# Kernel optimization log

Hardware: AMD Instinct MI355X
Metric: run time of the kernel (lower is better)

Reference implementation:

```python
import jax, jax.numpy as jnp
import numpy as np

N = 100000
E = 1600000
D_IN = 128
D_OUT = 128
D_DEC = 2
TAU = 0.5
NEG_SLOPE = 0.2  # PyG GATv2Conv default negative_slope


def _glorot(key, shape):
    lim = (6.0 / (shape[0] + shape[1])) ** 0.5
    return jax.random.uniform(key, shape, jnp.float32, -lim, lim)


def gatv2(x, edge_index, Wl, Wr, bl, br, att, bias):
    """PyG GATv2Conv, heads=1, add_self_loops=True, eval mode (no dropout).
    out[i] = sum_j softmax_i( att . leaky_relu(xl[j] + xr[i]) ) * xl[j] + bias
    """
    n = x.shape[0]
    loops = jnp.arange(n, dtype=edge_index.dtype)
    src = jnp.concatenate([edge_index[0], loops])  # [E+N]
    dst = jnp.concatenate([edge_index[1], loops])
    xl = x @ Wl + bl  # [N, out]
    xr = x @ Wr + br
    # per-edge unnormalized score
    e = jax.nn.leaky_relu(xl[src] + xr[dst], NEG_SLOPE) @ att  # [E+N]
    # scatter-softmax over incoming edges of each target node
    m = jax.ops.segment_max(e, dst, num_segments=n)
    a = jnp.exp(e - m[dst])
    s = jax.ops.segment_sum(a, dst, num_segments=n)
    alpha = a / (s[dst] + 1e-16)
    out = jax.ops.segment_sum(alpha[:, None] * xl[src], dst, num_segments=n)
    return out + bias


def setup_inputs() -> dict:
    key = jax.random.key(0)
    ks = jax.random.split(key, 16)
    x = jax.random.normal(ks[0], (N, D_IN), jnp.float32)
    edge_dec = jax.random.randint(ks[1], (2, E), 0, N, jnp.int64)
    edge_0 = jax.random.randint(ks[2], (2, E), 0, N, jnp.int64)
    edge_1 = jax.random.randint(ks[3], (2, E), 0, N, jnp.int64)
    u = jax.random.uniform(ks[4], (N, D_DEC), jnp.float32, 1e-6, 1.0 - 1e-6)
    gumbel = -jnp.log(-jnp.log(u))  # Gumbel(0,1) noise
    # shared GAT (used for every decision branch)
    Wl_g = _glorot(ks[5], (D_IN, D_OUT))
    Wr_g = _glorot(ks[6], (D_IN, D_OUT))
    bl_g = jnp.zeros((D_OUT,), jnp.float32)
    br_g = jnp.zeros((D_OUT,), jnp.float32)
    att_g = _glorot(ks[7], (D_OUT, 1))[:, 0]
    bias_g = jnp.zeros((D_OUT,), jnp.float32)
    # decision GAT
    Wl_d = _glorot(ks[8], (D_IN, D_DEC))
    Wr_d = _glorot(ks[9], (D_IN, D_DEC))
    bl_d = jnp.zeros((D_DEC,), jnp.float32)
    br_d = jnp.zeros((D_DEC,), jnp.float32)
    att_d = _glorot(ks[10], (D_DEC, 1))[:, 0]
    bias_d = jnp.zeros((D_DEC,), jnp.float32)
    return {"x": x, "edge_dec": edge_dec, "edge_0": edge_0, "edge_1": edge_1,
            "gumbel": gumbel,
            "Wl_g": Wl_g, "Wr_g": Wr_g, "bl_g": bl_g, "br_g": br_g,
            "att_g": att_g, "bias_g": bias_g,
            "Wl_d": Wl_d, "Wr_d": Wr_d, "bl_d": bl_d, "br_d": br_d,
            "att_d": att_d, "bias_d": bias_d}


def reference(x, edge_dec, edge_0, edge_1, gumbel,
              Wl_g, Wr_g, bl_g, br_g, att_g, bias_g,
              Wl_d, Wr_d, bl_d, br_d, att_d, bias_d):
    # decision logits via decision GAT on the decision edge set
    logits = gatv2(x, edge_dec, Wl_d, Wr_d, bl_d, br_d, att_d, bias_d)  # [N, 2]
    # hard gumbel-softmax with straight-through estimator, tau=0.5
    y_soft = jax.nn.softmax((logits + gumbel) / TAU, axis=-1)
    idx = jnp.argmax(y_soft, axis=-1)
    y_hard = jax.nn.one_hot(idx, y_soft.shape[-1], dtype=y_soft.dtype)
    decisions = y_hard + y_soft - jax.lax.stop_gradient(y_soft)
    # per-decision GAT (shared weights, different edge sets), gated sum
    out = jnp.zeros((x.shape[0], Wl_g.shape[1]), x.dtype)
    for i, ei in enumerate([edge_0, edge_1]):
        out = out + gatv2(x, ei, Wl_g, Wr_g, bl_g, br_g, att_g, bias_g) * decisions[:, i:i + 1]
    return out
```

## Files before the change

kernel.cpp:

```cpp
#include <hip/hip_runtime.h>

#define NEG 0.2f
#define CAPD 1792
#define CAPC 2816
#define CH 32768
#define NBMAX 1600

typedef __attribute__((ext_vector_type(8))) short short8;
typedef __attribute__((ext_vector_type(4))) float f32x4;

static __device__ __forceinline__ unsigned short f2bf(float f) {
  unsigned u = __float_as_uint(f);
  u += 0x7fffu + ((u >> 16) & 1u);
  return (unsigned short)(u >> 16);
}
static __device__ __forceinline__ float bflo(unsigned u) {
  return __uint_as_float(u << 16);
}
static __device__ __forceinline__ float bfhi(unsigned u) {
  return __uint_as_float(u & 0xffff0000u);
}
static __device__ __forceinline__ float bfx(const uint4& v, int f) {
  unsigned c = (f < 2) ? v.x : (f < 4) ? v.y : (f < 6) ? v.z : v.w;
  return (f & 1) ? bfhi(c) : bflo(c);
}
static __device__ __forceinline__ unsigned f2u(float f) {
  unsigned b = __float_as_uint(f);
  return (b & 0x80000000u) ? ~b : (b | 0x80000000u);
}
static __device__ __forceinline__ float u2f(unsigned u) {
  unsigned b = (u & 0x80000000u) ? (u ^ 0x80000000u) : ~u;
  return __uint_as_float(b);
}

__global__ void k_prep_wt(const float* __restrict__ Wl, const float* __restrict__ Wr,
                          unsigned short* __restrict__ wt) {
  int idx = blockIdx.x * 256 + threadIdx.x;
  int c = idx >> 7, k = idx & 127;
  float v = (c < 128) ? Wl[(size_t)k * 128 + c] : Wr[(size_t)k * 128 + (c - 128)];
  wt[idx] = f2bf(v);
}

__global__ __launch_bounds__(256) void k_gemm_main(
    const float* __restrict__ x, const unsigned short* __restrict__ wt,
    const float* __restrict__ bl, const float* __restrict__ br,
    const float* __restrict__ Wld, const float* __restrict__ Wrd,
    const float* __restrict__ bld, const float* __restrict__ brd,
    unsigned short* __restrict__ xl, unsigned short* __restrict__ xr,
    float* __restrict__ xld, float* __restrict__ xrd, int N) {
  int w = threadIdx.x >> 6, lane = threadIdx.x & 63;
  int m = lane & 15, quad = lane >> 4;
  int rowbase = blockIdx.x * 16;
  if (rowbase >= N) return;
  int colbase = w * 64;
  f32x4 acc[4] = {};
  float dl0 = 0.f, dl1 = 0.f, dr0 = 0.f, dr1 = 0.f;
  const float* arow = x + (size_t)(rowbase + m) * 128 + quad * 8;
#pragma unroll
  for (int kb = 0; kb < 128; kb += 32) {
    float4 a0 = *(const float4*)(arow + kb);
    float4 a1 = *(const float4*)(arow + kb + 4);
    if (w == 0) {
      int k0 = kb + quad * 8;
      const float4* wl4 = (const float4*)(Wld + 2 * k0);
      const float4* wr4 = (const float4*)(Wrd + 2 * k0);
      float4 l0 = wl4[0], l1 = wl4[1], l2 = wl4[2], l3 = wl4[3];
      float4 r0 = wr4[0], r1 = wr4[1], r2 = wr4[2], r3 = wr4[3];
      dl0 = fmaf(a0.x, l0.x, dl0); dl1 = fmaf(a0.x, l0.y, dl1);
      dl0 = fmaf(a0.y, l0.z, dl0); dl1 = fmaf(a0.y, l0.w, dl1);
      dl0 = fmaf(a0.z, l1.x, dl0); dl1 = fmaf(a0.z, l1.y, dl1);
      dl0 = fmaf(a0.w, l1.z, dl0); dl1 = fmaf(a0.w, l1.w, dl1);
      dl0 = fmaf(a1.x, l2.x, dl0); dl1 = fmaf(a1.x, l2.y, dl1);
      dl0 = fmaf(a1.y, l2.z, dl0); dl1 = fmaf(a1.y, l2.w, dl1);
      dl0 = fmaf(a1.z, l3.x, dl0); dl1 = fmaf(a1.z, l3.y, dl1);
      dl0 = fmaf(a1.w, l3.z, dl0); dl1 = fmaf(a1.w, l3.w, dl1);
      dr0 = fmaf(a0.x, r0.x, dr0); dr1 = fmaf(a0.x, r0.y, dr1);
      dr0 = fmaf(a0.y, r0.z, dr0); dr1 = fmaf(a0.y, r0.w, dr1);
      dr0 = fmaf(a0.z, r1.x, dr0); dr1 = fmaf(a0.z, r1.y, dr1);
      dr0 = fmaf(a0.w, r1.z, dr0); dr1 = fmaf(a0.w, r1.w, dr1);
      dr0 = fmaf(a1.x, r2.x, dr0); dr1 = fmaf(a1.x, r2.y, dr1);
      dr0 = fmaf(a1.y, r2.z, dr0); dr1 = fmaf(a1.y, r2.w, dr1);
      dr0 = fmaf(a1.z, r3.x, dr0); dr1 = fmaf(a1.z, r3.y, dr1);
      dr0 = fmaf(a1.w, r3.z, dr0); dr1 = fmaf(a1.w, r3.w, dr1);
    }
    short8 af;
    af[0] = (short)f2bf(a0.x); af[1] = (short)f2bf(a0.y);
    af[2] = (short)f2bf(a0.z); af[3] = (short)f2bf(a0.w);
    af[4] = (short)f2bf(a1.x); af[5] = (short)f2bf(a1.y);
    af[6] = (short)f2bf(a1.z); af[7] = (short)f2bf(a1.w);
#pragma unroll
    for (int ct = 0; ct < 4; ct++) {
      const unsigned short* bp =
          wt + (size_t)(colbase + ct * 16 + m) * 128 + kb + quad * 8;
      short8 bfr = *(const short8*)bp;
      acc[ct] = __builtin_amdgcn_mfma_f32_16x16x32_bf16(af, bfr, acc[ct], 0, 0, 0);
    }
  }
  if (w == 0) {
    dl0 += __shfl_xor(dl0, 16); dl0 += __shfl_xor(dl0, 32);
    dl1 += __shfl_xor(dl1, 16); dl1 += __shfl_xor(dl1, 32);
    dr0 += __shfl_xor(dr0, 16); dr0 += __shfl_xor(dr0, 32);
    dr1 += __shfl_xor(dr1, 16); dr1 += __shfl_xor(dr1, 32);
    if (quad == 0) {
      int row = rowbase + m;
      float2 vl; vl.x = dl0 + bld[0]; vl.y = dl1 + bld[1];
      float2 vr; vr.x = dr0 + brd[0]; vr.y = dr1 + brd[1];
      *(float2*)(xld + 2 * (size_t)row) = vl;
      *(float2*)(xrd + 2 * (size_t)row) = vr;
    }
  }
#pragma unroll
  for (int ct = 0; ct < 4; ct++) {
    int c = colbase + ct * 16 + m;
    float badd = (c < 128) ? bl[c] : br[c - 128];
#pragma unroll
    for (int r = 0; r < 4; r++) {
      int row = rowbase + quad * 4 + r;
      unsigned short v = f2bf(acc[ct][r] + badd);
      if (c < 128) xl[(size_t)row * 128 + c] = v;
      else         xr[(size_t)row * 128 + (c - 128)] = v;
    }
  }
}

__global__ void k_zero(int* __restrict__ gcur, int n) {
  int i = blockIdx.x * 256 + threadIdx.x;
  if (i < n) gcur[i] = 0;
}

__global__ __launch_bounds__(1024) void k_bin_all(
    const int* __restrict__ ed, const int* __restrict__ e0,
    const int* __restrict__ e1, int* __restrict__ gcur_d,
    int* __restrict__ gcur_c, unsigned* __restrict__ bind,
    unsigned* __restrict__ binc, long E, int NB) {
  __shared__ int hd[NBMAX], hc[NBMAX];
  int tid = threadIdx.x;
  long base = (long)blockIdx.x * CH;
  long T = 3 * E;
  for (int b = tid; b < NB; b += 1024) { hd[b] = 0; hc[b] = 0; }
  __syncthreads();
  for (int i = 0; i < CH / 1024; i++) {
    long idx = base + i * 1024 + tid;
    if (idx < T) {
      if (idx < E) {
        atomicAdd(&hd[ed[E + idx] >> 6], 1);
      } else {
        const int* L = (idx < 2 * E) ? e0 : e1;
        long j = (idx < 2 * E) ? idx - E : idx - 2 * E;
        atomicAdd(&hc[L[E + j] >> 6], 1);
      }
    }
  }
  __syncthreads();
  for (int b = tid; b < NB; b += 1024) {
    int cd = hd[b];
    hd[b] = cd ? atomicAdd(&gcur_d[b], cd) : 0;
    int cc = hc[b];
    hc[b] = cc ? atomicAdd(&gcur_c[b], cc) : 0;
  }
  __syncthreads();
  for (int i = 0; i < CH / 1024; i++) {
    long idx = base + i * 1024 + tid;
    if (idx < T) {
      if (idx < E) {
        int s = ed[idx], t = ed[E + idx];
        int b = t >> 6;
        int pos = atomicAdd(&hd[b], 1);
        if (pos < CAPD)
          bind[(size_t)b * CAPD + pos] = ((unsigned)s << 6) | (unsigned)(t & 63);
      } else {
        int k = idx >= 2 * E;
        const int* L = k ? e1 : e0;
        long j = idx - E - (k ? E : 0);
        int s = L[j], t = L[E + j];
        int b = t >> 6;
        int pos = atomicAdd(&hc[b], 1);
        if (pos < CAPC)
          binc[(size_t)b * CAPC + pos] =
              ((unsigned)s << 7) | ((unsigned)k << 6) | (unsigned)(t & 63);
      }
    }
  }
}

__global__ __launch_bounds__(256) void k_fused(
    const unsigned* __restrict__ bind, const unsigned* __restrict__ binc,
    const int* __restrict__ gcur_d, const int* __restrict__ gcur_c,
    const unsigned short* __restrict__ xl, const unsigned short* __restrict__ xr,
    const float* __restrict__ xld, const float* __restrict__ xrd,
    const float* __restrict__ attd, const float* __restrict__ biasd,
    const float* __restrict__ g, const float* __restrict__ att,
    const float* __restrict__ bias, float* __restrict__ out, int N) {
  __shared__ float xrd_s[128];
  __shared__ unsigned nmax[64];
  __shared__ float nsum[64], na0[64], na1[64];
  __shared__ int dec_s[64], scnt[64];
  __shared__ int slots[64 * 65];
  int tid = threadIdx.x;
  int b = blockIdx.x, nb0 = b << 6;
  int cntd = gcur_d[b]; if (cntd > CAPD) cntd = CAPD;
  int cntc = gcur_c[b]; if (cntc > CAPC) cntc = CAPC;
  float a0 = attd[0], a1 = attd[1];
  float eself = 0.f, x0s = 0.f, x1s = 0.f;
  int node = nb0 + tid;
  if (tid < 64) {
    if (node < N) {
      float2 xrv = *(const float2*)(xrd + 2 * (size_t)node);
      xrd_s[2 * tid] = xrv.x; xrd_s[2 * tid + 1] = xrv.y;
      float2 xlv = *(const float2*)(xld + 2 * (size_t)node);
      x0s = xlv.x; x1s = xlv.y;
      float h0 = x0s + xrv.x, h1 = x1s + xrv.y;
      eself = a0 * fmaxf(h0, NEG * h0) + a1 * fmaxf(h1, NEG * h1);
      nmax[tid] = f2u(eself);
    } else {
      xrd_s[2 * tid] = 0.f; xrd_s[2 * tid + 1] = 0.f;
      nmax[tid] = f2u(0.f);
    }
    nsum[tid] = 0.f; na0[tid] = 0.f; na1[tid] = 0.f;
  }
  __syncthreads();
  const unsigned* bd = bind + (size_t)b * CAPD;
  const float2* xld2 = (const float2*)xld;
  auto dscore = [&](float2 v, int tl) {
    float h0 = v.x + xrd_s[2 * tl], h1 = v.y + xrd_s[2 * tl + 1];
    return a0 * fmaxf(h0, NEG * h0) + a1 * fmaxf(h1, NEG * h1);
  };
  int cld = cntd - 1; if (cld < 0) cld = 0;
  for (int i = tid; i < cntd; i += 1024) {
    int i1 = min(i + 256, cld), i2 = min(i + 512, cld), i3 = min(i + 768, cld);
    unsigned pk0 = bd[i], pk1 = bd[i1], pk2 = bd[i2], pk3 = bd[i3];
    float2 v0 = xld2[pk0 >> 6], v1 = xld2[pk1 >> 6];
    float2 v2 = xld2[pk2 >> 6], v3 = xld2[pk3 >> 6];
    atomicMax(&nmax[pk0 & 63], f2u(dscore(v0, pk0 & 63)));
    if (i + 256 < cntd) atomicMax(&nmax[pk1 & 63], f2u(dscore(v1, pk1 & 63)));
    if (i + 512 < cntd) atomicMax(&nmax[pk2 & 63], f2u(dscore(v2, pk2 & 63)));
    if (i + 768 < cntd) atomicMax(&nmax[pk3 & 63], f2u(dscore(v3, pk3 & 63)));
  }
  __syncthreads();
  for (int i = tid; i < cntd; i += 1024) {
    int i1 = min(i + 256, cld), i2 = min(i + 512, cld), i3 = min(i + 768, cld);
    unsigned pk0 = bd[i], pk1 = bd[i1], pk2 = bd[i2], pk3 = bd[i3];
    float2 v0 = xld2[pk0 >> 6], v1 = xld2[pk1 >> 6];
    float2 v2 = xld2[pk2 >> 6], v3 = xld2[pk3 >> 6];
    {
      int tl = pk0 & 63;
      float w = expf(dscore(v0, tl) - u2f(nmax[tl]));
      atomicAdd(&nsum[tl], w); atomicAdd(&na0[tl], w * v0.x); atomicAdd(&na1[tl], w * v0.y);
    }
    if (i + 256 < cntd) {
      int tl = pk1 & 63;
      float w = expf(dscore(v1, tl) - u2f(nmax[tl]));
      atomicAdd(&nsum[tl], w); atomicAdd(&na0[tl], w * v1.x); atomicAdd(&na1[tl], w * v1.y);
    }
    if (i + 512 < cntd) {
      int tl = pk2 & 63;
      float w = expf(dscore(v2, tl) - u2f(nmax[tl]));
      atomicAdd(&nsum[tl], w); atomicAdd(&na0[tl], w * v2.x); atomicAdd(&na1[tl], w * v2.y);
    }
    if (i + 768 < cntd) {
      int tl = pk3 & 63;
      float w = expf(dscore(v3, tl) - u2f(nmax[tl]));
      atomicAdd(&nsum[tl], w); atomicAdd(&na0[tl], w * v3.x); atomicAdd(&na1[tl], w * v3.y);
    }
  }
  __syncthreads();
  if (tid < 64) {
    if (node < N) {
      float mm = u2f(nmax[tid]);
      float ws = expf(eself - mm);
      float den = nsum[tid] + ws + 1e-16f;
      float z0 = (na0[tid] + ws * x0s) / den + biasd[0] + g[2 * (size_t)node];
      float z1 = (na1[tid] + ws * x1s) / den + biasd[1] + g[2 * (size_t)node + 1];
      dec_s[tid] = (z1 > z0) ? 1 : 0;
      scnt[tid] = 1; slots[tid * 65] = node;
    } else {
      dec_s[tid] = -1; scnt[tid] = 0; slots[tid * 65] = 0;
    }
  }
  __syncthreads();
  const unsigned* bc = binc + (size_t)b * CAPC;
  for (int i = tid; i < cntc; i += 256) {
    unsigned pk = bc[i];
    int tl = pk & 63, k = (pk >> 6) & 1;
    if (k == dec_s[tl]) {
      int pos = atomicAdd(&scnt[tl], 1);
      if (pos < 64) slots[tl * 65 + pos] = pk >> 7;
    }
  }
  __syncthreads();

  int lane = tid & 63, l = lane & 15, gg = tid >> 4;
  const float4* at4 = (const float4*)att;
  float4 atA = at4[l * 2], atB = at4[l * 2 + 1];
  float atv[8] = {atA.x, atA.y, atA.z, atA.w, atB.x, atB.y, atB.z, atB.w};
  const float4* b4 = (const float4*)bias;
  float4 bA = b4[l * 2], bB = b4[l * 2 + 1];

  for (int rep = 0; rep < 4; rep++) {
    int nn = rep * 16 + gg;
    int nd = nb0 + nn;
    bool nvalid = nd < N;
    int cnt = scnt[nn]; if (cnt > 64) cnt = 64;
    if (!nvalid) cnt = 0;
    int mc = max(cnt, __shfl_xor(cnt, 16));
    mc = max(mc, __shfl_xor(mc, 32));

    int nc = nvalid ? nd : 0;
    uint4 xrp = ((const uint4*)(xr + (size_t)nc * 128))[l];
    float xrv[8] = {bflo(xrp.x), bfhi(xrp.x), bflo(xrp.y), bfhi(xrp.y),
                    bflo(xrp.z), bfhi(xrp.z), bflo(xrp.w), bfhi(xrp.w)};

    int cl = cnt - 1; if (cl < 0) cl = 0;
    const int* srow = &slots[nn * 65];
    uint4 cur[4];
#pragma unroll
    for (int j = 0; j < 4; j++) {
      int idx = j > cl ? cl : j;
      cur[j] = ((const uint4*)(xl + (size_t)srow[idx] * 128))[l];
    }
    float m = -3.0e38f, lsum = 0.f;
    float gacc[8] = {0.f, 0.f, 0.f, 0.f, 0.f, 0.f, 0.f, 0.f};

    for (int e = 0; e < mc; e += 4) {
      uint4 nxt[4];
#pragma unroll
      for (int j = 0; j < 4; j++) {
        int idx = e + 4 + j; if (idx > cl) idx = cl;
        nxt[j] = ((const uint4*)(xl + (size_t)srow[idx] * 128))[l];
      }
      float p[4];
#pragma unroll
      for (int j = 0; j < 4; j++) {
        float pj = 0.f;
#pragma unroll
        for (int f = 0; f < 8; f++) {
          float h = bfx(cur[j], f) + xrv[f];
          pj = fmaf(atv[f], fmaxf(h, NEG * h), pj);
        }
        p[j] = pj;
      }
#pragma unroll
      for (int off = 1; off < 16; off <<= 1) {
        p[0] += __shfl_xor(p[0], off); p[1] += __shfl_xor(p[1], off);
        p[2] += __shfl_xor(p[2], off); p[3] += __shfl_xor(p[3], off);
      }
      float pe0 = (e     < cnt) ? p[0] : -3.0e38f;
      float pe1 = (e + 1 < cnt) ? p[1] : -3.0e38f;
      float pe2 = (e + 2 < cnt) ? p[2] : -3.0e38f;
      float pe3 = (e + 3 < cnt) ? p[3] : -3.0e38f;
      float nm = fmaxf(m, fmaxf(fmaxf(pe0, pe1), fmaxf(pe2, pe3)));
      float sc = __expf(m - nm);
      float w0 = __expf(pe0 - nm), w1 = __expf(pe1 - nm);
      float w2 = __expf(pe2 - nm), w3 = __expf(pe3 - nm);
      lsum = lsum * sc + w0 + w1 + w2 + w3;
#pragma unroll
      for (int f = 0; f < 8; f++) {
        float t0 = fmaf(w0, bfx(cur[0], f), gacc[f] * sc);
        float t1 = fmaf(w1, bfx(cur[1], f), t0);
        float t2 = fmaf(w2, bfx(cur[2], f), t1);
        gacc[f]  = fmaf(w3, bfx(cur[3], f), t2);
      }
      m = nm;
#pragma unroll
      for (int j = 0; j < 4; j++) cur[j] = nxt[j];
    }
    if (nvalid) {
      float inv = 1.0f / (lsum + 1e-16f);
      float4 oA, oB;
      oA.x = gacc[0] * inv + bA.x; oA.y = gacc[1] * inv + bA.y;
      oA.z = gacc[2] * inv + bA.z; oA.w = gacc[3] * inv + bA.w;
      oB.x = gacc[4] * inv + bB.x; oB.y = gacc[5] * inv + bB.y;
      oB.z = gacc[6] * inv + bB.z; oB.w = gacc[7] * inv + bB.w;
      float4* op = (float4*)(out + (size_t)nd * 128 + l * 8);
      op[0] = oA; op[1] = oB;
    }
  }
}

extern "C" void kernel_launch(void* const* d_in, const int* in_sizes, int n_in,
                              void* d_out, int out_size, void* d_ws, size_t ws_size,
                              hipStream_t stream) {
  const float* x      = (const float*)d_in[0];
  const int*   ed     = (const int*)d_in[1];
  const int*   e0     = (const int*)d_in[2];
  const int*   e1     = (const int*)d_in[3];
  const float* gumbel = (const float*)d_in[4];
  const float* Wl_g   = (const float*)d_in[5];
  const float* Wr_g   = (const float*)d_in[6];
  const float* bl_g   = (const float*)d_in[7];
  const float* br_g   = (const float*)d_in[8];
  const float* att_g  = (const float*)d_in[9];
  const float* bias_g = (const float*)d_in[10];
  const float* Wl_d   = (const float*)d_in[11];
  const float* Wr_d   = (const float*)d_in[12];
  const float* bl_d   = (const float*)d_in[13];
  const float* br_d   = (const float*)d_in[14];
  const float* att_d  = (const float*)d_in[15];
  const float* bias_d = (const float*)d_in[16];

  const int  N  = in_sizes[0] / 128;
  const long E  = in_sizes[1] / 2;
  const int  NB = (N + 63) / 64;

  char* p = (char*)d_ws;
  auto alloc = [&](size_t bytes) -> void* {
    void* r = (void*)p;
    p += (bytes + 255) & ~(size_t)255;
    return r;
  };
  unsigned short* xl = (unsigned short*)alloc((size_t)N * 128 * 2);
  unsigned short* xr = (unsigned short*)alloc((size_t)N * 128 * 2);
  unsigned short* wt = (unsigned short*)alloc((size_t)256 * 128 * 2);
  float* xld     = (float*)alloc((size_t)N * 2 * 4);
  float* xrd     = (float*)alloc((size_t)N * 2 * 4);
  int* gcur      = (int*)alloc((size_t)2 * NB * 4);
  unsigned* bind = (unsigned*)alloc((size_t)NB * CAPD * 4);
  unsigned* binc = (unsigned*)alloc((size_t)NB * CAPC * 4);
  int* gcur_d = gcur, * gcur_c = gcur + NB;

  const int gB  = (int)((3 * E + CH - 1) / CH);
  const int gZ  = (2 * NB + 255) / 256;

  k_prep_wt<<<128, 256, 0, stream>>>(Wl_g, Wr_g, wt);
  k_gemm_main<<<(N + 15) / 16, 256, 0, stream>>>(x, wt, bl_g, br_g, Wl_d, Wr_d,
                                                 bl_d, br_d, xl, xr, xld, xrd, N);
  k_zero<<<gZ, 256, 0, stream>>>(gcur, 2 * NB);
  k_bin_all<<<gB, 1024, 0, stream>>>(ed, e0, e1, gcur_d, gcur_c, bind, binc, E, NB);
  k_fused<<<NB, 256, 0, stream>>>(bind, binc, gcur_d, gcur_c, xl, xr, xld, xrd,
                                  att_d, bias_d, gumbel, att_g, bias_g,
                                  (float*)d_out, N);
}
```

Baseline: 456.5 us.

## Stage binned edges in LDS via block counting sort before global writes

The edge binning kernel now does a per-block counting sort. It builds a histogram, runs an exclusive scan in shared memory and scatters the payloads into an LDS staging buffer grouped by bin. It then copies each bin's run to its reserved global slot range, so global writes land in contiguous runs instead of one atomic-indexed scattered store per edge. The chunk size drops and the block size changes to fit the staging buffer in LDS, which means more blocks and more global reservation atomics. The separate counter-zeroing kernel is also folded into the weight-prep kernel to save a launch.

```diff
diff --git a/kernel.cpp b/kernel.cpp
--- a/kernel.cpp
+++ b/kernel.cpp
@@ -3,8 +3,11 @@
 #define NEG 0.2f
 #define CAPD 1792
 #define CAPC 2816
-#define CH 32768
+#define CH 9216
+#define NT 512
 #define NBMAX 1600
+#define HTOT 3584
+#define K 7
 
 typedef __attribute__((ext_vector_type(8))) short short8;
 typedef __attribute__((ext_vector_type(4))) float f32x4;
@@ -34,11 +37,17 @@
 }
 
 __global__ void k_prep_wt(const float* __restrict__ Wl, const float* __restrict__ Wr,
-                          unsigned short* __restrict__ wt) {
-  int idx = blockIdx.x * 256 + threadIdx.x;
-  int c = idx >> 7, k = idx & 127;
-  float v = (c < 128) ? Wl[(size_t)k * 128 + c] : Wr[(size_t)k * 128 + (c - 128)];
-  wt[idx] = f2bf(v);
+                          unsigned short* __restrict__ wt, int* __restrict__ gcur,
+                          int ncur) {
+  if (blockIdx.x < 128) {
+    int idx = blockIdx.x * 256 + threadIdx.x;
+    int c = idx >> 7, k = idx & 127;
+    float v = (c < 128) ? Wl[(size_t)k * 128 + c] : Wr[(size_t)k * 128 + (c - 128)];
+    wt[idx] = f2bf(v);
+  } else {
+    int i = (blockIdx.x - 128) * 256 + threadIdx.x;
+    if (i < ncur) gcur[i] = 0;
+  }
 }
 
 __global__ __launch_bounds__(256) void k_gemm_main(
@@ -123,61 +132,103 @@
   }
 }
 
-__global__ void k_zero(int* __restrict__ gcur, int n) {
-  int i = blockIdx.x * 256 + threadIdx.x;
-  if (i < n) gcur[i] = 0;
-}
-
-__global__ __launch_bounds__(1024) void k_bin_all(
+__global__ __launch_bounds__(NT) void k_bin_all(
     const int* __restrict__ ed, const int* __restrict__ e0,
     const int* __restrict__ e1, int* __restrict__ gcur_d,
     int* __restrict__ gcur_c, unsigned* __restrict__ bind,
     unsigned* __restrict__ binc, long E, int NB) {
-  __shared__ int hd[NBMAX], hc[NBMAX];
+  __shared__ unsigned stage[CH];
+  __shared__ int h[HTOT + 1];
+  __shared__ int gbase[HTOT];
+  __shared__ int wtot[8], wexcl[8];
   int tid = threadIdx.x;
   long base = (long)blockIdx.x * CH;
   long T = 3 * E;
-  for (int b = tid; b < NB; b += 1024) { hd[b] = 0; hc[b] = 0; }
-  __syncthreads();
-  for (int i = 0; i < CH / 1024; i++) {
-    long idx = base + i * 1024 + tid;
+  for (int a = tid; a < HTOT + 1; a += NT) h[a] = 0;
+  __syncthreads();
+  for (int it = 0; it < CH / NT; it++) {
+    long idx = base + it * NT + tid;
     if (idx < T) {
-      if (idx < E) {
-        atomicAdd(&hd[ed[E + idx] >> 6], 1);
-      } else {
-        const int* L = (idx < 2 * E) ? e0 : e1;
-        long j = (idx < 2 * E) ? idx - E : idx - 2 * E;
-        atomicAdd(&hc[L[E + j] >> 6], 1);
-      }
-    }
-  }
-  __syncthreads();
-  for (int b = tid; b < NB; b += 1024) {
-    int cd = hd[b];
-    hd[b] = cd ? atomicAdd(&gcur_d[b], cd) : 0;
-    int cc = hc[b];
-    hc[b] = cc ? atomicAdd(&gcur_c[b], cc) : 0;
-  }
-  __syncthreads();
-  for (int i = 0; i < CH / 1024; i++) {
-    long idx = base + i * 1024 + tid;
+      int ha;
+      if (idx < E) ha = ed[E + idx] >> 6;
+      else if (idx < 2 * E) ha = NBMAX + (e0[E + idx - E] >> 6);
+      else ha = NBMAX + (e1[E + idx - 2 * E] >> 6);
+      atomicAdd(&h[ha], 1);
+    }
+  }
+  __syncthreads();
+  {
+    int vals[K];
+    int bi = tid * K, tot = 0;
+#pragma unroll
+    for (int k = 0; k < K; k++) { vals[k] = h[bi + k]; tot += vals[k]; }
+    int lane = tid & 63, wv = tid >> 6;
+    int inc = tot;
+    for (int off = 1; off < 64; off <<= 1) {
+      int nv = __shfl_up(inc, off);
+      if (lane >= off) inc += nv;
+    }
+    if (lane == 63) wtot[wv] = inc;
+    __syncthreads();
+    if (tid == 0) {
+      int r = 0;
+      for (int wwi = 0; wwi < 8; wwi++) { wexcl[wwi] = r; r += wtot[wwi]; }
+    }
+    __syncthreads();
+    int run = wexcl[wv] + (inc - tot);
+#pragma unroll
+    for (int k = 0; k < K; k++) { int v = vals[k]; h[bi + k] = run; run += v; }
+    if (tid == NT - 1) h[HTOT] = run;
+  }
+  __syncthreads();
+  for (int a = tid; a < HTOT; a += NT) {
+    int cnt = h[a + 1] - h[a];
+    if (cnt > 0) {
+      if (a < NBMAX) { if (a < NB) gbase[a] = atomicAdd(&gcur_d[a], cnt); }
+      else if (a < 2 * NBMAX) {
+        int b = a - NBMAX;
+        if (b < NB) gbase[a] = atomicAdd(&gcur_c[b], cnt);
+      }
+    }
+  }
+  __syncthreads();
+  for (int it = 0; it < CH / NT; it++) {
+    long idx = base + it * NT + tid;
     if (idx < T) {
+      int ha; unsigned pay;
       if (idx < E) {
         int s = ed[idx], t = ed[E + idx];
-        int b = t >> 6;
-        int pos = atomicAdd(&hd[b], 1);
-        if (pos < CAPD)
-          bind[(size_t)b * CAPD + pos] = ((unsigned)s << 6) | (unsigned)(t & 63);
+        ha = t >> 6;
+        pay = ((unsigned)s << 6) | (unsigned)(t & 63);
       } else {
         int k = idx >= 2 * E;
         const int* L = k ? e1 : e0;
         long j = idx - E - (k ? E : 0);
         int s = L[j], t = L[E + j];
-        int b = t >> 6;
-        int pos = atomicAdd(&hc[b], 1);
-        if (pos < CAPC)
-          binc[(size_t)b * CAPC + pos] =
-              ((unsigned)s << 7) | ((unsigned)k << 6) | (unsigned)(t & 63);
+        ha = NBMAX + (t >> 6);
+        pay = ((unsigned)s << 7) | ((unsigned)k << 6) | (unsigned)(t & 63);
+      }
+      int pos = atomicAdd(&h[ha], 1);
+      stage[pos] = pay;
+    }
+  }
+  __syncthreads();
+  for (int a = tid; a < HTOT; a += NT) {
+    int start = a ? h[a - 1] : 0;
+    int end = h[a];
+    if (end <= start) continue;
+    int gb = gbase[a];
+    if (a < NBMAX) {
+      unsigned* dst = bind + (size_t)a * CAPD;
+      for (int i = start; i < end; i++) {
+        int o = gb + (i - start);
+        if (o < CAPD) dst[o] = stage[i];
+      }
+    } else if (a < 2 * NBMAX) {
+      unsigned* dst = binc + (size_t)(a - NBMAX) * CAPC;
+      for (int i = start; i < end; i++) {
+        int o = gb + (i - start);
+        if (o < CAPC) dst[o] = stage[i];
       }
     }
   }
@@ -418,14 +469,13 @@
   unsigned* binc = (unsigned*)alloc((size_t)NB * CAPC * 4);
   int* gcur_d = gcur, * gcur_c = gcur + NB;
 
-  const int gB  = (int)((3 * E + CH - 1) / CH);
-  const int gZ  = (2 * NB + 255) / 256;
-
-  k_prep_wt<<<128, 256, 0, stream>>>(Wl_g, Wr_g, wt);
+  const int gB = (int)((3 * E + CH - 1) / CH);
+  const int gZ = (2 * NB + 255) / 256;
+
+  k_prep_wt<<<128 + gZ, 256, 0, stream>>>(Wl_g, Wr_g, wt, gcur, 2 * NB);
   k_gemm_main<<<(N + 15) / 16, 256, 0, stream>>>(x, wt, bl_g, br_g, Wl_d, Wr_d,
                                                  bl_d, br_d, xl, xr, xld, xrd, N);
-  k_zero<<<gZ, 256, 0, stream>>>(gcur, 2 * NB);
-  k_bin_all<<<gB, 1024, 0, stream>>>(ed, e0, e1, gcur_d, gcur_c, bind, binc, E, NB);
+  k_bin_all<<<gB, NT, 0, stream>>>(ed, e0, e1, gcur_d, gcur_c, bind, binc, E, NB);
   k_fused<<<NB, 256, 0, stream>>>(bind, binc, gcur_d, gcur_c, xl, xr, xld, xrd,
                                   att_d, bias_d, gumbel, att_g, bias_g,
                                   (float*)d_out, N);
```

Result: faster. 422.7 us (-7.4%).
